# Optimization experiments

Measured on AMD Instinct MI355X. Metric: run time of the kernel, lower is better.

Reference implementation:

```python
import jax, jax.numpy as jnp
import numpy as np

B, S, D = 4, 2048, 1024
N_EXPERTS, EXPERT_SIZE = 16, 256
WIDTH = N_EXPERTS * EXPERT_SIZE  # 4096


def setup_inputs() -> dict:
    key = jax.random.key(0)
    k_x, k_w1, k_w2, k_g = jax.random.split(key, 4)
    x = jax.random.normal(k_x, (B, S, D), dtype=jnp.float32)
    # Linear params, fan-in scaled init
    w1 = jax.random.normal(k_w1, (D, WIDTH), dtype=jnp.float32) / np.sqrt(D).astype(np.float32)
    b1 = jnp.zeros((WIDTH,), dtype=jnp.float32)
    w2 = jax.random.normal(k_w2, (WIDTH, D), dtype=jnp.float32) / np.sqrt(WIDTH).astype(np.float32)
    b2 = jnp.zeros((D,), dtype=jnp.float32)
    return {"x": x, "w1": w1, "b1": b1, "w2": w2, "b2": b2}


def reference(x, w1, b1, w2, b2):
    # NOTE: the original module computes expert-choice routing tensors
    # (gate einsum -> topk -> one_hot -> identity matmul 'gather'), but the
    # returned value is ONLY the dense FFN applied to x; all routing results
    # are dead code with no effect on the output. Faithful output math:
    h = jax.nn.relu(jnp.einsum('bsd,dw->bsw', x, w1) + b1)  # [B,S,WIDTH]
    return jnp.einsum('bsw,wd->bsd', h, w2) + b2            # [B,S,D]
```

## Files before the change

### kernel.cpp

```cpp
#include <hip/hip_runtime.h>
#include <hip/hip_bf16.h>


typedef __bf16 bf16;
typedef __bf16 bf16x4 __attribute__((ext_vector_type(4)));
typedef __bf16 bf16x8 __attribute__((ext_vector_type(8)));
typedef float  f32x4  __attribute__((ext_vector_type(4)));

#define BM 128
#define BN 128
#define BK 64

__device__ __forceinline__ void gload_lds16(const bf16* g, bf16* l) {
    __builtin_amdgcn_global_load_lds(
        (const __attribute__((address_space(1))) unsigned int*)g,
        (__attribute__((address_space(3))) unsigned int*)l,
        16, 0, 0);
}

__device__ __forceinline__ void transpose_tile(
    const float* __restrict__ in, bf16* __restrict__ out,
    int K, int N, int k0, int n0, int t, bf16 (*tile)[72])
{
    const int lr = t >> 4;
    const int lc = (t & 15) << 2;
#pragma unroll
    for (int p = 0; p < 4; ++p) {
        int k = p * 16 + lr;
        float4 v = *(const float4*)(in + (size_t)(k0 + k) * N + n0 + lc);
        tile[lc + 0][k] = (bf16)v.x;
        tile[lc + 1][k] = (bf16)v.y;
        tile[lc + 2][k] = (bf16)v.z;
        tile[lc + 3][k] = (bf16)v.w;
    }
    __syncthreads();

    const int wr = t >> 3;
    const int wc = (t & 7) << 3;
#pragma unroll
    for (int p = 0; p < 2; ++p) {
        int n = p * 32 + wr;
        *(bf16x8*)(out + (size_t)(n0 + n) * K + k0 + wc) =
            *(const bf16x8*)&tile[n][wc];
    }
}

__global__ __launch_bounds__(256) void prep_fused(
    const float* __restrict__ x,  bf16* __restrict__ xb,
    const float* __restrict__ w1, bf16* __restrict__ w1t,
    const float* __restrict__ w2, bf16* __restrict__ w2t)
{
    __shared__ __align__(16) bf16 tile[64][72];
    const int bid = blockIdx.x;
    const int t   = threadIdx.x;

    if (bid < 8192) {
        int i = bid * 256 + t;
        float4 v = ((const float4*)x)[i];
        bf16x4 o;
        o.x = (bf16)v.x; o.y = (bf16)v.y; o.z = (bf16)v.z; o.w = (bf16)v.w;
        ((bf16x4*)xb)[i] = o;
    } else if (bid < 9216) {
        int b = bid - 8192;
        transpose_tile(w1, w1t, 1024, 4096, (b >> 6) * 64, (b & 63) * 64, t, tile);
    } else {
        int b = bid - 9216;
        transpose_tile(w2, w2t, 4096, 1024, (b >> 4) * 64, (b & 15) * 64, t, tile);
    }
}

template <int FUSE_RELU_BF16>
__global__ __launch_bounds__(256, 3) void gemm_bt(
    const bf16* __restrict__ A, const bf16* __restrict__ Bt,
    const float* __restrict__ bias, void* __restrict__ Cout,
    int M, int N, int K)
{
    __shared__ __align__(16) bf16 As[BM * BK];
    __shared__ __align__(16) bf16 Bs[BN * BK];

    const int tid  = threadIdx.x;
    const int wave = tid >> 6;
    const int lane = tid & 63;

    const int l8  = lane >> 3;
    const int c8  = lane & 7;
    const int swc = (c8 ^ l8) << 3;
    const size_t K_ = (size_t)K;

    const bf16* gA[4]; const bf16* gB[4];
    bf16* lA[4]; bf16* lB[4];
#pragma unroll
    for (int g = 0; g < 4; ++g) {
        const int rr = wave * 32 + g * 8 + l8;
        gA[g] = A  + ((size_t)blockIdx.y * BM + rr) * K_ + swc;
        gB[g] = Bt + ((size_t)blockIdx.x * BN + rr) * K_ + swc;
        lA[g] = &As[(wave * 32 + g * 8) * BK] + lane * 8;
        lB[g] = &Bs[(wave * 32 + g * 8) * BK] + lane * 8;
    }

    const int wm   = (wave >> 1) << 6;
    const int wn   = (wave & 1) << 6;
    const int quad = lane >> 4;
    const int r    = lane & 15;
    const int r7   = lane & 7;

    f32x4 acc[4][4] = {};

    for (int k0 = 0; k0 < K; k0 += BK) {
        __syncthreads();
#pragma unroll
        for (int g = 0; g < 4; ++g) {
            gload_lds16(gA[g], lA[g]);
            gload_lds16(gB[g], lB[g]);
            gA[g] += BK; gB[g] += BK;
        }
        __syncthreads();

#pragma unroll
        for (int h = 0; h < 2; ++h) {
            const int ch = ((h * 4 + quad) ^ r7) << 3;
            bf16x8 af[4], bfr[4];
#pragma unroll
            for (int i = 0; i < 4; ++i)
                af[i] = *(const bf16x8*)&As[(wm + i * 16 + r) * BK + ch];
#pragma unroll
            for (int j = 0; j < 4; ++j)
                bfr[j] = *(const bf16x8*)&Bs[(wn + j * 16 + r) * BK + ch];
#pragma unroll
            for (int i = 0; i < 4; ++i)
#pragma unroll
                for (int j = 0; j < 4; ++j)
                    acc[i][j] = __builtin_amdgcn_mfma_f32_16x16x32_bf16(
                        af[i], bfr[j], acc[i][j], 0, 0, 0);
        }
    }

    const int m_base = blockIdx.y * BM + wm + quad * 4;
    const int n_base = blockIdx.x * BN + wn + r;
    float bv[4];
#pragma unroll
    for (int j = 0; j < 4; ++j) bv[j] = bias[n_base + j * 16];

    if (FUSE_RELU_BF16) {
        bf16* Cb = (bf16*)Cout;
#pragma unroll
        for (int i = 0; i < 4; ++i) {
#pragma unroll
            for (int p = 0; p < 4; ++p) {
                size_t row = (size_t)(m_base + i * 16 + p) * (size_t)N;
#pragma unroll
                for (int j = 0; j < 4; ++j) {
                    float v = acc[i][j][p] + bv[j];
                    v = v > 0.f ? v : 0.f;
                    Cb[row + n_base + j * 16] = (bf16)v;
                }
            }
        }
    } else {
        float* Cf = (float*)Cout;
#pragma unroll
        for (int i = 0; i < 4; ++i) {
#pragma unroll
            for (int p = 0; p < 4; ++p) {
                size_t row = (size_t)(m_base + i * 16 + p) * (size_t)N;
#pragma unroll
                for (int j = 0; j < 4; ++j) {
                    Cf[row + n_base + j * 16] = acc[i][j][p] + bv[j];
                }
            }
        }
    }
}

__global__ __launch_bounds__(256, 2) void gemm_bt2_k128(
    const bf16* __restrict__ A, const bf16* __restrict__ Bt,
    const float* __restrict__ bias, float* __restrict__ Cf,
    int M, int N, int K)
{
    __shared__ __align__(16) bf16 As[128 * 128];
    __shared__ __align__(16) bf16 Bs[128 * 128];

    const int tid  = threadIdx.x;
    const int wave = tid >> 6;
    const int lane = tid & 63;

    const int sr   = tid >> 4;
    const int swc  = ((tid & 15) ^ sr) << 3;
    const size_t K_ = (size_t)K;

    const bf16* gA[8]; const bf16* gB[8];
    bf16* lA[8]; bf16* lB[8];
#pragma unroll
    for (int g = 0; g < 8; ++g) {
        const int rr = g * 16 + sr;
        gA[g] = A  + ((size_t)blockIdx.y * 128 + rr) * K_ + swc;
        gB[g] = Bt + ((size_t)blockIdx.x * 128 + rr) * K_ + swc;
        lA[g] = &As[(g * 16) * 128] + tid * 8;
        lB[g] = &Bs[(g * 16) * 128] + tid * 8;
    }

    const int wm   = (wave >> 1) << 6;
    const int wn   = (wave & 1) << 6;
    const int quad = lane >> 4;
    const int r    = lane & 15;

    f32x4 acc[4][4] = {};

    for (int k0 = 0; k0 < K; k0 += 128) {
        __syncthreads();
#pragma unroll
        for (int g = 0; g < 8; ++g) {
            gload_lds16(gA[g], lA[g]);
            gload_lds16(gB[g], lB[g]);
            gA[g] += 128; gB[g] += 128;
        }
        __syncthreads();

#pragma unroll
        for (int ks = 0; ks < 4; ++ks) {
            bf16x8 af[4], bfr[4];
#pragma unroll
            for (int i = 0; i < 4; ++i) {
                const int row = wm + i * 16 + r;
                const int ch  = (((ks * 4 + quad) ^ (row & 15)) << 3);
                af[i] = *(const bf16x8*)&As[row * 128 + ch];
            }
#pragma unroll
            for (int j = 0; j < 4; ++j) {
                const int row = wn + j * 16 + r;
                const int ch  = (((ks * 4 + quad) ^ (row & 15)) << 3);
                bfr[j] = *(const bf16x8*)&Bs[row * 128 + ch];
            }
#pragma unroll
            for (int i = 0; i < 4; ++i)
#pragma unroll
                for (int j = 0; j < 4; ++j)
                    acc[i][j] = __builtin_amdgcn_mfma_f32_16x16x32_bf16(
                        af[i], bfr[j], acc[i][j], 0, 0, 0);
        }
    }

    const int m_base = blockIdx.y * 128 + wm + quad * 4;
    const int n_base = blockIdx.x * 128 + wn + r;
    float bv[4];
#pragma unroll
    for (int j = 0; j < 4; ++j) bv[j] = bias[n_base + j * 16];

#pragma unroll
    for (int i = 0; i < 4; ++i) {
#pragma unroll
        for (int p = 0; p < 4; ++p) {
            size_t row = (size_t)(m_base + i * 16 + p) * (size_t)N;
#pragma unroll
            for (int j = 0; j < 4; ++j) {
                Cf[row + n_base + j * 16] = acc[i][j][p] + bv[j];
            }
        }
    }
}

extern "C" void kernel_launch(void* const* d_in, const int* in_sizes, int n_in,
                              void* d_out, int out_size, void* d_ws, size_t ws_size,
                              hipStream_t stream)
{
    const float* x  = (const float*)d_in[0];
    const float* w1 = (const float*)d_in[1];
    const float* b1 = (const float*)d_in[2];
    const float* w2 = (const float*)d_in[3];
    const float* b2 = (const float*)d_in[4];
    float* out = (float*)d_out;

    const int M = 8192, D = 1024, W = 4096;

    char* ws = (char*)d_ws;
    bf16* xb  = (bf16*)(ws);
    bf16* w1t = (bf16*)(ws + (size_t)(16 << 20));
    bf16* w2t = (bf16*)(ws + (size_t)(24 << 20));
    bf16* h   = (bf16*)(ws + (size_t)(32 << 20));

    prep_fused<<<10240, 256, 0, stream>>>(x, xb, w1, w1t, w2, w2t);

    gemm_bt<1><<<dim3(W / BN, M / BM), 256, 0, stream>>>(
        xb, w1t, b1, (void*)h, M, W, D);

    gemm_bt2_k128<<<dim3(D / 128, M / 128), 256, 0, stream>>>(
        h, w2t, b2, out, M, D, W);
}
```

Baseline: 249.4 us.

## Move w2 transpose into first GEMM launch as extra blocks

The w2 fp32-to-bf16 transpose moves out of the prep kernel and runs as 1024 extra trailing blocks of the first GEMM grid, reusing its LDS. The intent is to let this memory-bound work overlap with the compute-bound GEMM tail. The first GEMM grid is flattened to 1D with manual tile indexing. The x conversion now uses fewer blocks, each handling 4 float4s, which cuts block-launch overhead in the prep kernel. Risks: the transpose blocks have to wait until GEMM blocks free CU slots, and they run under the GEMM's launch bounds.

Result: no change. 252.0 us (+1.0%).

```diff
diff --git a/kernel.cpp b/kernel.cpp
--- a/kernel.cpp
+++ b/kernel.cpp
@@ -47,25 +47,25 @@
 
 __global__ __launch_bounds__(256) void prep_fused(
     const float* __restrict__ x,  bf16* __restrict__ xb,
-    const float* __restrict__ w1, bf16* __restrict__ w1t,
-    const float* __restrict__ w2, bf16* __restrict__ w2t)
+    const float* __restrict__ w1, bf16* __restrict__ w1t)
 {
     __shared__ __align__(16) bf16 tile[64][72];
     const int bid = blockIdx.x;
     const int t   = threadIdx.x;
 
-    if (bid < 8192) {
-        int i = bid * 256 + t;
-        float4 v = ((const float4*)x)[i];
-        bf16x4 o;
-        o.x = (bf16)v.x; o.y = (bf16)v.y; o.z = (bf16)v.z; o.w = (bf16)v.w;
-        ((bf16x4*)xb)[i] = o;
-    } else if (bid < 9216) {
-        int b = bid - 8192;
+    if (bid < 2048) {
+        int base = bid * 256 + t;
+#pragma unroll
+        for (int it = 0; it < 4; ++it) {
+            int i = base + it * (2048 * 256);
+            float4 v = ((const float4*)x)[i];
+            bf16x4 o;
+            o.x = (bf16)v.x; o.y = (bf16)v.y; o.z = (bf16)v.z; o.w = (bf16)v.w;
+            ((bf16x4*)xb)[i] = o;
+        }
+    } else {
+        int b = bid - 2048;
         transpose_tile(w1, w1t, 1024, 4096, (b >> 6) * 64, (b & 63) * 64, t, tile);
-    } else {
-        int b = bid - 9216;
-        transpose_tile(w2, w2t, 4096, 1024, (b >> 4) * 64, (b & 15) * 64, t, tile);
     }
 }
 
@@ -73,12 +73,24 @@
 __global__ __launch_bounds__(256, 3) void gemm_bt(
     const bf16* __restrict__ A, const bf16* __restrict__ Bt,
     const float* __restrict__ bias, void* __restrict__ Cout,
-    int M, int N, int K)
+    int M, int N, int K,
+    const float* __restrict__ w2, bf16* __restrict__ w2t, int nGemm)
 {
     __shared__ __align__(16) bf16 As[BM * BK];
     __shared__ __align__(16) bf16 Bs[BN * BK];
 
-    const int tid  = threadIdx.x;
+    const int bid = blockIdx.x;
+    const int tid = threadIdx.x;
+
+    if (bid >= nGemm) {
+        int b = bid - nGemm;
+        transpose_tile(w2, w2t, 4096, 1024, (b >> 4) * 64, (b & 15) * 64,
+                       tid, (bf16(*)[72])As);
+        return;
+    }
+    const int tx = bid & 31;
+    const int ty = bid >> 5;
+
     const int wave = tid >> 6;
     const int lane = tid & 63;
 
@@ -92,8 +104,8 @@
 #pragma unroll
     for (int g = 0; g < 4; ++g) {
         const int rr = wave * 32 + g * 8 + l8;
-        gA[g] = A  + ((size_t)blockIdx.y * BM + rr) * K_ + swc;
-        gB[g] = Bt + ((size_t)blockIdx.x * BN + rr) * K_ + swc;
+        gA[g] = A  + ((size_t)ty * BM + rr) * K_ + swc;
+        gB[g] = Bt + ((size_t)tx * BN + rr) * K_ + swc;
         lA[g] = &As[(wave * 32 + g * 8) * BK] + lane * 8;
         lB[g] = &Bs[(wave * 32 + g * 8) * BK] + lane * 8;
     }
@@ -135,8 +147,8 @@
         }
     }
 
-    const int m_base = blockIdx.y * BM + wm + quad * 4;
-    const int n_base = blockIdx.x * BN + wn + r;
+    const int m_base = ty * BM + wm + quad * 4;
+    const int n_base = tx * BN + wn + r;
     float bv[4];
 #pragma unroll
     for (int j = 0; j < 4; ++j) bv[j] = bias[n_base + j * 16];
@@ -278,10 +290,10 @@
     bf16* w2t = (bf16*)(ws + (size_t)(24 << 20));
     bf16* h   = (bf16*)(ws + (size_t)(32 << 20));
 
-    prep_fused<<<10240, 256, 0, stream>>>(x, xb, w1, w1t, w2, w2t);
-
-    gemm_bt<1><<<dim3(W / BN, M / BM), 256, 0, stream>>>(
-        xb, w1t, b1, (void*)h, M, W, D);
+    prep_fused<<<3072, 256, 0, stream>>>(x, xb, w1, w1t);
+
+    gemm_bt<1><<<2048 + 1024, 256, 0, stream>>>(
+        xb, w1t, b1, (void*)h, M, W, D, w2, w2t, 2048);
 
     gemm_bt2_k128<<<dim3(D / 128, M / 128), 256, 0, stream>>>(
         h, w2t, b2, out, M, D, W);
```

## Replace first GEMM with triple-buffered 256x128 pipelined kernel

Applied to the files above, without the earlier changes.

Swaps the first GEMM (x·w1 + bias, ReLU, bf16 output) for a new 512-thread kernel using 256x128 tiles and a three-stage LDS ring buffer. Direct-to-LDS global loads for the next stages are interleaved with the MFMA work, the wait uses a partial vmcnt, and MFMA sections run at raised wave priority. The goal is to hide global-load latency and drop one of the two barriers per K step that the old kernel needed. In exchange it uses much more LDS (one block per CU) and more accumulator registers, and gives a coarser grid.

Measured after the change: 262.7 us. +5.3%, slower.

```diff
diff --git a/kernel.cpp b/kernel.cpp
--- a/kernel.cpp
+++ b/kernel.cpp
@@ -7,9 +7,8 @@
 typedef __bf16 bf16x8 __attribute__((ext_vector_type(8)));
 typedef float  f32x4  __attribute__((ext_vector_type(4)));
 
-#define BM 128
-#define BN 128
-#define BK 64
+#define G1_ASZ (256 * 64)
+#define G1_BSZ (128 * 64)
 
 __device__ __forceinline__ void gload_lds16(const bf16* g, bf16* l) {
     __builtin_amdgcn_global_load_lds(
@@ -69,104 +68,144 @@
     }
 }
 
-template <int FUSE_RELU_BF16>
-__global__ __launch_bounds__(256, 3) void gemm_bt(
+__global__ __launch_bounds__(512, 1) void gemm1_pipe(
     const bf16* __restrict__ A, const bf16* __restrict__ Bt,
-    const float* __restrict__ bias, void* __restrict__ Cout,
+    const float* __restrict__ bias, bf16* __restrict__ Cb,
     int M, int N, int K)
 {
-    __shared__ __align__(16) bf16 As[BM * BK];
-    __shared__ __align__(16) bf16 Bs[BN * BK];
+    __shared__ __align__(16) bf16 As[3 * G1_ASZ];
+    __shared__ __align__(16) bf16 Bs[3 * G1_BSZ];
 
     const int tid  = threadIdx.x;
     const int wave = tid >> 6;
     const int lane = tid & 63;
-
-    const int l8  = lane >> 3;
-    const int c8  = lane & 7;
-    const int swc = (c8 ^ l8) << 3;
+    const int tx   = blockIdx.x;
+    const int ty   = blockIdx.y;
     const size_t K_ = (size_t)K;
 
-    const bf16* gA[4]; const bf16* gB[4];
-    bf16* lA[4]; bf16* lB[4];
-#pragma unroll
-    for (int g = 0; g < 4; ++g) {
-        const int rr = wave * 32 + g * 8 + l8;
-        gA[g] = A  + ((size_t)blockIdx.y * BM + rr) * K_ + swc;
-        gB[g] = Bt + ((size_t)blockIdx.x * BN + rr) * K_ + swc;
-        lA[g] = &As[(wave * 32 + g * 8) * BK] + lane * 8;
-        lB[g] = &Bs[(wave * 32 + g * 8) * BK] + lane * 8;
-    }
-
-    const int wm   = (wave >> 1) << 6;
-    const int wn   = (wave & 1) << 6;
+    const int srow = tid >> 3;
+    const int swc  = ((tid & 7) ^ (srow & 7)) << 3;
+    const bf16* gA[4]; const bf16* gB[2];
+#pragma unroll
+    for (int g = 0; g < 4; ++g)
+        gA[g] = A + ((size_t)ty * 256 + g * 64 + srow) * K_ + swc;
+#pragma unroll
+    for (int g = 0; g < 2; ++g)
+        gB[g] = Bt + ((size_t)tx * 128 + g * 64 + srow) * K_ + swc;
+    const int ldsOff = tid * 8;
+
+    const int wm   = (wave >> 2) * 128;
+    const int wn   = (wave & 3) * 32;
     const int quad = lane >> 4;
     const int r    = lane & 15;
     const int r7   = lane & 7;
 
-    f32x4 acc[4][4] = {};
-
-    for (int k0 = 0; k0 < K; k0 += BK) {
-        __syncthreads();
-#pragma unroll
-        for (int g = 0; g < 4; ++g) {
-            gload_lds16(gA[g], lA[g]);
-            gload_lds16(gB[g], lB[g]);
-            gA[g] += BK; gB[g] += BK;
-        }
-        __syncthreads();
-
-#pragma unroll
-        for (int h = 0; h < 2; ++h) {
-            const int ch = ((h * 4 + quad) ^ r7) << 3;
-            bf16x8 af[4], bfr[4];
-#pragma unroll
-            for (int i = 0; i < 4; ++i)
-                af[i] = *(const bf16x8*)&As[(wm + i * 16 + r) * BK + ch];
-#pragma unroll
-            for (int j = 0; j < 4; ++j)
-                bfr[j] = *(const bf16x8*)&Bs[(wn + j * 16 + r) * BK + ch];
-#pragma unroll
-            for (int i = 0; i < 4; ++i)
-#pragma unroll
-                for (int j = 0; j < 4; ++j)
-                    acc[i][j] = __builtin_amdgcn_mfma_f32_16x16x32_bf16(
-                        af[i], bfr[j], acc[i][j], 0, 0, 0);
-        }
-    }
-
-    const int m_base = blockIdx.y * BM + wm + quad * 4;
-    const int n_base = blockIdx.x * BN + wn + r;
-    float bv[4];
-#pragma unroll
-    for (int j = 0; j < 4; ++j) bv[j] = bias[n_base + j * 16];
-
-    if (FUSE_RELU_BF16) {
-        bf16* Cb = (bf16*)Cout;
-#pragma unroll
-        for (int i = 0; i < 4; ++i) {
-#pragma unroll
-            for (int p = 0; p < 4; ++p) {
-                size_t row = (size_t)(m_base + i * 16 + p) * (size_t)N;
-#pragma unroll
-                for (int j = 0; j < 4; ++j) {
-                    float v = acc[i][j][p] + bv[j];
-                    v = v > 0.f ? v : 0.f;
-                    Cb[row + n_base + j * 16] = (bf16)v;
-                }
-            }
-        }
-    } else {
-        float* Cf = (float*)Cout;
-#pragma unroll
-        for (int i = 0; i < 4; ++i) {
-#pragma unroll
-            for (int p = 0; p < 4; ++p) {
-                size_t row = (size_t)(m_base + i * 16 + p) * (size_t)N;
-#pragma unroll
-                for (int j = 0; j < 4; ++j) {
-                    Cf[row + n_base + j * 16] = acc[i][j][p] + bv[j];
-                }
+    f32x4 acc[8][2] = {};
+    const int NT = K >> 6;
+
+#pragma unroll
+    for (int g = 0; g < 4; ++g) { gload_lds16(gA[g], &As[0 * G1_ASZ + g * 4096 + ldsOff]); gA[g] += 64; }
+#pragma unroll
+    for (int g = 0; g < 2; ++g) { gload_lds16(gB[g], &Bs[0 * G1_BSZ + g * 4096 + ldsOff]); gB[g] += 64; }
+#pragma unroll
+    for (int g = 0; g < 4; ++g) { gload_lds16(gA[g], &As[1 * G1_ASZ + g * 4096 + ldsOff]); gA[g] += 64; }
+#pragma unroll
+    for (int g = 0; g < 2; ++g) { gload_lds16(gB[g], &Bs[1 * G1_BSZ + g * 4096 + ldsOff]); gB[g] += 64; }
+    asm volatile("s_waitcnt vmcnt(6)" ::: "memory");
+    __builtin_amdgcn_s_barrier();
+    asm volatile("" ::: "memory");
+
+    int cur = 0;
+    for (int t = 0; t < NT; ++t) {
+        const int nb = (cur + 2 >= 3) ? cur - 1 : cur + 2;
+        const bf16* Ac = &As[cur * G1_ASZ];
+        const bf16* Bc = &Bs[cur * G1_BSZ];
+        bf16* An = &As[nb * G1_ASZ];
+        bf16* Bn = &Bs[nb * G1_BSZ];
+        const bool st = (t + 2 < NT);
+
+        bf16x8 af[4][2], bfr[2][2];
+#pragma unroll
+        for (int i = 0; i < 4; ++i)
+#pragma unroll
+            for (int h = 0; h < 2; ++h)
+                af[i][h] = *(const bf16x8*)&Ac[(wm + i * 16 + r) * 64 +
+                                               (((h * 4 + quad) ^ r7) << 3)];
+#pragma unroll
+        for (int j = 0; j < 2; ++j)
+#pragma unroll
+            for (int h = 0; h < 2; ++h)
+                bfr[j][h] = *(const bf16x8*)&Bc[(wn + j * 16 + r) * 64 +
+                                                (((h * 4 + quad) ^ r7) << 3)];
+        if (st) {
+            gload_lds16(gA[0], An + 0 * 4096 + ldsOff);
+            gload_lds16(gA[1], An + 1 * 4096 + ldsOff);
+            gload_lds16(gA[2], An + 2 * 4096 + ldsOff);
+        }
+        __builtin_amdgcn_s_setprio(1);
+#pragma unroll
+        for (int i = 0; i < 4; ++i)
+#pragma unroll
+            for (int j = 0; j < 2; ++j) {
+                acc[i][j] = __builtin_amdgcn_mfma_f32_16x16x32_bf16(
+                    af[i][0], bfr[j][0], acc[i][j], 0, 0, 0);
+                acc[i][j] = __builtin_amdgcn_mfma_f32_16x16x32_bf16(
+                    af[i][1], bfr[j][1], acc[i][j], 0, 0, 0);
+            }
+        __builtin_amdgcn_s_setprio(0);
+
+        bf16x8 ag[4][2];
+#pragma unroll
+        for (int i = 0; i < 4; ++i)
+#pragma unroll
+            for (int h = 0; h < 2; ++h)
+                ag[i][h] = *(const bf16x8*)&Ac[(wm + 64 + i * 16 + r) * 64 +
+                                               (((h * 4 + quad) ^ r7) << 3)];
+        if (st) {
+            gload_lds16(gA[3], An + 3 * 4096 + ldsOff);
+            gload_lds16(gB[0], Bn + 0 * 4096 + ldsOff);
+            gload_lds16(gB[1], Bn + 1 * 4096 + ldsOff);
+#pragma unroll
+            for (int g = 0; g < 4; ++g) gA[g] += 64;
+#pragma unroll
+            for (int g = 0; g < 2; ++g) gB[g] += 64;
+        }
+        __builtin_amdgcn_s_setprio(1);
+#pragma unroll
+        for (int i = 0; i < 4; ++i)
+#pragma unroll
+            for (int j = 0; j < 2; ++j) {
+                acc[i + 4][j] = __builtin_amdgcn_mfma_f32_16x16x32_bf16(
+                    ag[i][0], bfr[j][0], acc[i + 4][j], 0, 0, 0);
+                acc[i + 4][j] = __builtin_amdgcn_mfma_f32_16x16x32_bf16(
+                    ag[i][1], bfr[j][1], acc[i + 4][j], 0, 0, 0);
+            }
+        __builtin_amdgcn_s_setprio(0);
+
+        if (st) { asm volatile("s_waitcnt vmcnt(6)" ::: "memory"); }
+        else    { asm volatile("s_waitcnt vmcnt(0)" ::: "memory"); }
+        __builtin_amdgcn_s_barrier();
+        asm volatile("" ::: "memory");
+
+        cur = (cur == 2) ? 0 : cur + 1;
+    }
+
+    const int m_base = ty * 256 + wm + quad * 4;
+    const int n_base = tx * 128 + wn + r;
+    float bv[2];
+#pragma unroll
+    for (int j = 0; j < 2; ++j) bv[j] = bias[n_base + j * 16];
+
+#pragma unroll
+    for (int i = 0; i < 8; ++i) {
+#pragma unroll
+        for (int p = 0; p < 4; ++p) {
+            size_t row = (size_t)(m_base + i * 16 + p) * (size_t)N;
+#pragma unroll
+            for (int j = 0; j < 2; ++j) {
+                float v = acc[i][j][p] + bv[j];
+                v = v > 0.f ? v : 0.f;
+                Cb[row + n_base + j * 16] = (bf16)v;
             }
         }
     }
@@ -280,8 +319,8 @@
 
     prep_fused<<<10240, 256, 0, stream>>>(x, xb, w1, w1t, w2, w2t);
 
-    gemm_bt<1><<<dim3(W / BN, M / BM), 256, 0, stream>>>(
-        xb, w1t, b1, (void*)h, M, W, D);
+    gemm1_pipe<<<dim3(W / 128, M / 256), 512, 0, stream>>>(
+        xb, w1t, b1, h, M, W, D);
 
     gemm_bt2_k128<<<dim3(D / 128, M / 128), 256, 0, stream>>>(
         h, w2t, b2, out, M, D, W);
```
